# Kernel tuning notes

Hardware: AMD Instinct MI355X
Metric: run time of the kernel (lower is better)

The kernel has to match this reference:

```python
import jax, jax.numpy as jnp
from jax import lax
import numpy as np

BN_EPS = 1e-5

def nearest_resize(x, out_h, out_w):
    # torch F.interpolate(mode='nearest'): src = floor(dst * in / out)
    B, C, H, W = x.shape
    hi = (jnp.arange(out_h) * H) // out_h
    wi = (jnp.arange(out_w) * W) // out_w
    return x[:, :, hi][:, :, :, wi]

def conv1x1(x, w, b=None):
    y = jnp.einsum('bchw,oc->bohw', x, w)
    if b is not None:
        y = y + b[None, :, None, None]
    return y

def dwconv(x, w, stride, pad):
    C = x.shape[1]
    return lax.conv_general_dilated(x, w, (stride, stride), [(pad, pad), (pad, pad)],
                                    dimension_numbers=('NCHW', 'OIHW', 'NCHW'),
                                    feature_group_count=C)

def bn(x, g, b, m, v):
    scale = g / jnp.sqrt(v + BN_EPS)
    return (x - m[None, :, None, None]) * scale[None, :, None, None] + b[None, :, None, None]


def setup_inputs() -> dict:
    key = jax.random.key(0)
    ks = jax.random.split(key, 8)
    B, C, H0, W0 = 4, 512, 192, 192
    w_scale = 0.05
    return {
        'x': jax.random.normal(ks[0], (B, C, H0, W0), jnp.float32),
        'q_w': jax.random.normal(ks[1], (C, C), jnp.float32) * w_scale,
        'q_b': jnp.zeros((C,), jnp.float32),
        'kv_w': jax.random.normal(ks[2], (2 * C, C), jnp.float32) * w_scale,
        'kv_b': jnp.zeros((2 * C,), jnp.float32),
        'sr1_w': jax.random.normal(ks[3], (C, 1, 2, 2), jnp.float32) * w_scale,
        'bn1_g': jnp.ones((C,), jnp.float32),
        'bn1_b': jnp.zeros((C,), jnp.float32),
        'bn1_m': jnp.zeros((C,), jnp.float32),
        'bn1_v': jnp.ones((C,), jnp.float32),
        'sr2_w': jax.random.normal(ks[4], (C, C), jnp.float32) * w_scale,
        'bn2_g': jnp.ones((C,), jnp.float32),
        'bn2_b': jnp.zeros((C,), jnp.float32),
        'bn2_m': jnp.zeros((C,), jnp.float32),
        'bn2_v': jnp.ones((C,), jnp.float32),
        'lc_w': jax.random.normal(ks[5], (C, 1, 3, 3), jnp.float32) * w_scale,
        'lc_b': jnp.zeros((C,), jnp.float32),
        'head_num': 8,
    }


def reference(x, q_w, q_b, kv_w, kv_b, sr1_w, bn1_g, bn1_b, bn1_m, bn1_v,
              sr2_w, bn2_g, bn2_b, bn2_m, bn2_v, lc_w, lc_b, head_num):
    origin_h, origin_w = x.shape[2], x.shape[3]
    x = nearest_resize(x, origin_h // 4, origin_w // 4)
    B, C, H, W = x.shape
    hd = C // head_num
    scale = hd ** (-0.5)

    # q projection (1x1 conv with bias)
    q = conv1x1(x, q_w, q_b)  # [B,C,H,W]

    # spatial reduction: depthwise conv(k=sr, s=sr, p=sr//2) + BN + ReLU, then 1x1 + BN
    sr = sr1_w.shape[-1]
    kv = jax.nn.relu(bn(dwconv(x, sr1_w, sr, sr // 2), bn1_g, bn1_b, bn1_m, bn1_v))
    kv = bn(conv1x1(kv, sr2_w), bn2_g, bn2_b, bn2_m, bn2_v)

    # local depthwise 3x3 conv residual
    kv = dwconv(kv, lc_w, 1, 1) + lc_b[None, :, None, None] + kv

    # kv projection (1x1 conv, 2C output)
    kv = conv1x1(kv, kv_w, kv_b)
    k, v = jnp.split(kv, 2, axis=1)  # each [B,C,Hs,Ws]
    M = k.shape[2] * k.shape[3]

    q_ = jnp.swapaxes(q.reshape(B, head_num, hd, H * W), -1, -2)  # [B,h,N,hd]
    k_ = k.reshape(B, head_num, hd, M)                             # [B,h,hd,M]
    v_ = jnp.swapaxes(v.reshape(B, head_num, hd, M), -1, -2)       # [B,h,M,hd]

    attn = jax.nn.softmax(jnp.matmul(q_, k_) * scale, axis=-1)     # [B,h,N,M]
    out = jnp.swapaxes(jnp.matmul(attn, v_), -1, -2).reshape(B, C, H, W)

    # NOTE: original torch code passes size=(origin_w, origin_h)
    out = nearest_resize(out, origin_w, origin_h)
    return out
```

## Files before the change

kernel.cpp:

```cpp
#include <hip/hip_runtime.h>

#define Bsz 4
#define Cc  512
#define C2  1024
#define H0c 192
#define Hh  48
#define Nn  2304
#define HNh 8
#define HD  64
#define Hs  25
#define Ms  625

typedef const float* fp;
typedef _Float16 f16;
typedef __attribute__((ext_vector_type(8))) _Float16 f16x8;
typedef __attribute__((ext_vector_type(4))) _Float16 f16x4;
typedef __attribute__((ext_vector_type(4))) float    f32x4;

__global__ __launch_bounds__(256) void k_front(
    fp __restrict__ x, f16* __restrict__ xt, f16* __restrict__ kv1t,
    fp __restrict__ w1, fp g, fp bb, fp bm, fp bv,
    fp __restrict__ q_w, fp __restrict__ sr2_w, fp __restrict__ kv_w,
    f16* __restrict__ wh)
{
    __shared__ float tile[32][33];
    const int t = threadIdx.x;
    int bid = blockIdx.x;

    if (bid < 4608) {
        const int b  = bid / 1152;
        const int yi = (bid / 72) % 16;
        const int xi = bid % 72;
        const int s0 = xi * 32, r0 = yi * 32;
        const float* xb = x + (size_t)b * Cc * H0c * H0c;
        #pragma unroll
        for (int p = 0; p < 4; p++) {
            int e = t + p * 256; int i = e >> 5, j = e & 31;
            int c = r0 + i, n = s0 + j;
            tile[i][j] = xb[((size_t)c * H0c + (n / Hh) * 4) * H0c + (n % Hh) * 4];
        }
        __syncthreads();
        #pragma unroll
        for (int p = 0; p < 4; p++) {
            int e = t + p * 256; int oi = e >> 5, oj = e & 31;
            xt[((size_t)b * Nn + s0 + oi) * Cc + r0 + oj] = (f16)tile[oj][oi];
        }
    } else if (bid < 5888) {
        bid -= 4608;
        const int b  = bid / 320;
        const int yi = (bid / 20) % 16;
        const int xi = bid % 20;
        const int s0 = xi * 32, r0 = yi * 32;
        #pragma unroll
        for (int p = 0; p < 4; p++) {
            int e = t + p * 256; int i = e >> 5, j = e & 31;
            int c = r0 + i, n = s0 + j;
            float v = 0.f;
            if (n < Ms) {
                int ho = n / Hs, wo = n % Hs;
                const float* src = x + (size_t)(b * Cc + c) * H0c * H0c;
                float acc = 0.f;
                #pragma unroll
                for (int di = 0; di < 2; di++) {
                    int ih = ho * 2 - 1 + di;
                    if (ih < 0 || ih >= Hh) continue;
                    #pragma unroll
                    for (int dj = 0; dj < 2; dj++) {
                        int iw = wo * 2 - 1 + dj;
                        if (iw < 0 || iw >= Hh) continue;
                        acc += w1[c * 4 + di * 2 + dj] * src[(size_t)(ih * 4) * H0c + iw * 4];
                    }
                }
                float sc = g[c] * rsqrtf(bv[c] + 1e-5f);
                v = fmaxf((acc - bm[c]) * sc + bb[c], 0.f);
            }
            tile[i][j] = v;
        }
        __syncthreads();
        #pragma unroll
        for (int p = 0; p < 4; p++) {
            int e = t + p * 256; int oi = e >> 5, oj = e & 31;
            if (s0 + oi < Ms)
                kv1t[((size_t)b * Ms + s0 + oi) * Cc + r0 + oj] = (f16)tile[oj][oi];
        }
    } else {
        bid -= 5888;
        int i4 = (bid * 256 + t) * 4;
        float4 v;
        if (i4 < 262144)      v = *(const float4*)&q_w[i4];
        else if (i4 < 524288) v = *(const float4*)&sr2_w[i4 - 262144];
        else                  v = *(const float4*)&kv_w[i4 - 524288];
        f16x4 h; h[0] = (f16)v.x; h[1] = (f16)v.y; h[2] = (f16)v.z; h[3] = (f16)v.w;
        *(f16x4*)&wh[i4] = h;
    }
}

__global__ __launch_bounds__(256) void k_lct(const float* __restrict__ kv2,
                                             fp __restrict__ w, fp __restrict__ lb,
                                             f16* __restrict__ kv3t) {
    __shared__ float tile[32][33];
    const int b = blockIdx.z;
    const int s0 = blockIdx.x * 32, r0 = blockIdx.y * 32;
    const int t = threadIdx.x;
    #pragma unroll
    for (int p = 0; p < 4; p++) {
        int e = t + p * 256; int i = e >> 5, j = e & 31;
        int c = r0 + i, n = s0 + j;
        float v = 0.f;
        if (n < Ms) {
            int ho = n / Hs, wo = n % Hs;
            const float* src = kv2 + ((size_t)b * Cc + c) * Ms;
            float acc = 0.f;
            #pragma unroll
            for (int di = 0; di < 3; di++) {
                int ih = ho - 1 + di;
                if (ih < 0 || ih >= Hs) continue;
                #pragma unroll
                for (int dj = 0; dj < 3; dj++) {
                    int iw = wo - 1 + dj;
                    if (iw < 0 || iw >= Hs) continue;
                    acc += w[c * 9 + di * 3 + dj] * src[ih * Hs + iw];
                }
            }
            v = acc + lb[c] + src[n];
        }
        tile[i][j] = v;
    }
    __syncthreads();
    #pragma unroll
    for (int p = 0; p < 4; p++) {
        int e = t + p * 256; int oi = e >> 5, oj = e & 31;
        if (s0 + oi < Ms)
            kv3t[((size_t)b * Ms + s0 + oi) * Cc + r0 + oj] = (f16)tile[oj][oi];
    }
}

__device__ __forceinline__ void gemm_body(
    const f16* __restrict__ W, const f16* __restrict__ Xt,
    float* __restrict__ Yf, f16* __restrict__ Yt, f16* __restrict__ Vt,
    const int Md, const int Nd, const int NtRows, const int mode, const float oscale,
    fp __restrict__ bias,
    fp __restrict__ bn_g, fp __restrict__ bn_b, fp __restrict__ bn_m, fp __restrict__ bn_v,
    const int bx, const int by, const int bz, f16* sA, f16* sB)
{
    const int b  = bz;
    const int m0 = by * 128, n0 = bx * 128;
    const int t = threadIdx.x;
    const int lane = t & 63, w = t >> 6;
    const int lm = lane & 15, q = lane >> 4;
    const int wm = w >> 1, wn = w & 1;
    const f16* Xb = Xt + (size_t)b * Nd * 512;

    f32x4 acc[4][4];
    #pragma unroll
    for (int i = 0; i < 4; i++)
        #pragma unroll
        for (int j = 0; j < 4; j++)
            #pragma unroll
            for (int r = 0; r < 4; r++) acc[i][j][r] = 0.f;

    for (int k0 = 0; k0 < 512; k0 += 64) {
        {
            int r = t >> 1, hh = (t & 1) * 32;
            const f16* wr = W + (size_t)(m0 + r) * 512 + k0 + hh;
            f16* dst = &sA[r * 80 + hh];
            #pragma unroll
            for (int i = 0; i < 4; i++)
                *(f16x8*)&dst[i * 8] = *(const f16x8*)&wr[i * 8];
        }
        {
            int r = t >> 1, hh = (t & 1) * 32;
            bool ok = (n0 + r) < Nd;
            const f16* xr = Xb + (size_t)(n0 + r) * 512 + k0 + hh;
            f16* dst = &sB[r * 80 + hh];
            #pragma unroll
            for (int i = 0; i < 4; i++) {
                f16x8 v;
                if (ok) {
                    v = *(const f16x8*)&xr[i * 8];
                } else {
                    for (int z = 0; z < 8; z++) v[z] = (f16)0.f;
                }
                *(f16x8*)&dst[i * 8] = v;
            }
        }
        __syncthreads();
        #pragma unroll
        for (int ks = 0; ks < 2; ks++) {
            f16x8 af[4], bf[4];
            #pragma unroll
            for (int i = 0; i < 4; i++)
                af[i] = *(const f16x8*)&sA[(wm * 64 + i * 16 + lm) * 80 + ks * 32 + q * 8];
            #pragma unroll
            for (int j = 0; j < 4; j++)
                bf[j] = *(const f16x8*)&sB[(wn * 64 + j * 16 + lm) * 80 + ks * 32 + q * 8];
            #pragma unroll
            for (int i = 0; i < 4; i++)
                #pragma unroll
                for (int j = 0; j < 4; j++)
                    acc[i][j] = __builtin_amdgcn_mfma_f32_16x16x32_f16(af[i], bf[j], acc[i][j], 0, 0, 0);
        }
        __syncthreads();
    }

    #pragma unroll
    for (int i = 0; i < 4; i++) {
        int ob = m0 + wm * 64 + i * 16 + q * 4;
        float badd[4], bsc[4], bsh[4];
        #pragma unroll
        for (int r = 0; r < 4; r++) {
            int o = ob + r;
            badd[r] = bias ? bias[o] : 0.f;
            if (bn_g) { bsc[r] = bn_g[o] * rsqrtf(bn_v[o] + 1e-5f); bsh[r] = bn_b[o] - bn_m[o] * bsc[r]; }
            else      { bsc[r] = 1.f; bsh[r] = 0.f; }
        }
        #pragma unroll
        for (int j = 0; j < 4; j++) {
            int n = n0 + wn * 64 + j * 16 + lm;
            f32x4 a = acc[i][j];
            if (mode == 0) {
                if (n < Nd) {
                    #pragma unroll
                    for (int r = 0; r < 4; r++)
                        Yf[((size_t)b * Md + ob + r) * Nd + n] = (a[r] + badd[r]) * bsc[r] + bsh[r];
                }
            } else if (mode == 1 || (mode == 2 && ob < 512)) {
                f16x4 h;
                #pragma unroll
                for (int r = 0; r < 4; r++) h[r] = (f16)((a[r] + badd[r]) * oscale);
                int hh = ob >> 6, d0 = ob & 63;
                *(f16x4*)&Yt[((size_t)(b * 8 + hh) * NtRows + n) * 64 + d0] = h;
            } else {
                #pragma unroll
                for (int r = 0; r < 4; r++) {
                    float val = (n < Nd) ? (a[r] + badd[r]) : 0.f;
                    Vt[((size_t)b * Cc + (ob + r - 512)) * 640 + n] = (f16)val;
                }
            }
        }
    }
}

__global__ __launch_bounds__(256) void k_gemm_mfma(
    const f16* __restrict__ W, const f16* __restrict__ Xt,
    float* __restrict__ Yf, f16* __restrict__ Yt, f16* __restrict__ Vt,
    const int Md, const int Nd, const int NtRows, const int mode, const float oscale,
    fp __restrict__ bias,
    fp __restrict__ bn_g, fp __restrict__ bn_b, fp __restrict__ bn_m, fp __restrict__ bn_v)
{
    __shared__ f16 sA[128 * 80];
    __shared__ f16 sB[128 * 80];
    gemm_body(W, Xt, Yf, Yt, Vt, Md, Nd, NtRows, mode, oscale,
              bias, bn_g, bn_b, bn_m, bn_v,
              blockIdx.x, blockIdx.y, blockIdx.z, sA, sB);
}

__global__ __launch_bounds__(256) void k_gemm2(
    const f16* __restrict__ W0, const f16* __restrict__ X0, f16* __restrict__ Yt0,
    const float osc0, fp __restrict__ bias0,
    const f16* __restrict__ W1, const f16* __restrict__ X1, float* __restrict__ Yf1,
    fp g1, fp b1, fp m1, fp v1)
{
    __shared__ f16 sA[128 * 80];
    __shared__ f16 sB[128 * 80];
    int bid = blockIdx.x;
    if (bid < 288) {
        int bx = bid % 18, by = (bid / 18) % 4, bz = bid / 72;
        gemm_body(W0, X0, nullptr, Yt0, nullptr, Cc, Nn, Nn, 1, osc0,
                  bias0, nullptr, nullptr, nullptr, nullptr, bx, by, bz, sA, sB);
    } else {
        bid -= 288;
        int bx = bid % 5, by = (bid / 5) % 4, bz = bid / 20;
        gemm_body(W1, X1, Yf1, nullptr, nullptr, Cc, Ms, 0, 0, 1.f,
                  nullptr, g1, b1, m1, v1, bx, by, bz, sA, sB);
    }
}

__global__ __launch_bounds__(256) void k_attn_mfma(
    const f16* __restrict__ Qt, const f16* __restrict__ Kt,
    const f16* __restrict__ Vt, float* __restrict__ Obuf)
{
    __shared__ f16 sK[64 * 80];
    __shared__ f16 sV[64 * 80];
    __shared__ f16 sP[4][16 * 80];

    int bh = blockIdx.y;
    int n0 = blockIdx.x * 64;
    int t = threadIdx.x, w = t >> 6, lane = t & 63;
    int lm = lane & 15, q = lane >> 4;
    f16* sPw = &sP[w][0];

    f16x8 qf[2];
    {
        const f16* qrow = Qt + ((size_t)bh * Nn + n0 + w * 16 + lm) * 64;
        qf[0] = *(const f16x8*)&qrow[q * 8];
        qf[1] = *(const f16x8*)&qrow[32 + q * 8];
    }

    f32x4 od[4];
    #pragma unroll
    for (int dt = 0; dt < 4; dt++)
        #pragma unroll
        for (int r = 0; r < 4; r++) od[dt][r] = 0.f;
    float mold[4], lold[4];
    #pragma unroll
    for (int r = 0; r < 4; r++) { mold[r] = -1e30f; lold[r] = 0.f; }

    int kr = t >> 2, kc = t & 3;
    const f16* kbase = Kt + (size_t)bh * 640 * 64;
    const f16* vbase = Vt + (size_t)bh * 64 * 640;

    for (int mc = 0; mc < 640; mc += 64) {
        {
            const f16* ksrc = kbase + (size_t)(mc + kr) * 64;
            *(f16x8*)&sK[kr * 80 + kc * 8]      = *(const f16x8*)&ksrc[kc * 8];
            *(f16x8*)&sK[kr * 80 + 32 + kc * 8] = *(const f16x8*)&ksrc[32 + kc * 8];
            const f16* vsrc = vbase + (size_t)kr * 640 + mc;
            *(f16x8*)&sV[kr * 80 + kc * 8]      = *(const f16x8*)&vsrc[kc * 8];
            *(f16x8*)&sV[kr * 80 + 32 + kc * 8] = *(const f16x8*)&vsrc[32 + kc * 8];
        }
        __syncthreads();

        f32x4 sc4[4];
        #pragma unroll
        for (int j = 0; j < 4; j++)
            #pragma unroll
            for (int r = 0; r < 4; r++) sc4[j][r] = 0.f;
        #pragma unroll
        for (int ks = 0; ks < 2; ks++) {
            #pragma unroll
            for (int j = 0; j < 4; j++) {
                f16x8 kf = *(const f16x8*)&sK[(j * 16 + lm) * 80 + ks * 32 + q * 8];
                sc4[j] = __builtin_amdgcn_mfma_f32_16x16x32_f16(qf[ks], kf, sc4[j], 0, 0, 0);
            }
        }

        const bool lastc = (mc >= 576);
        #pragma unroll
        for (int reg = 0; reg < 4; reg++) {
            float mx;
            if (lastc) {
                mx = -1e30f;
                #pragma unroll
                for (int j = 0; j < 4; j++) {
                    float s = sc4[j][reg];
                    if (576 + j * 16 + lm >= Ms) s = -1e30f;
                    sc4[j][reg] = s;
                    mx = fmaxf(mx, s);
                }
            } else {
                mx = fmaxf(fmaxf(sc4[0][reg], sc4[1][reg]),
                           fmaxf(sc4[2][reg], sc4[3][reg]));
            }
            #pragma unroll
            for (int off = 1; off < 16; off <<= 1) mx = fmaxf(mx, __shfl_xor(mx, off));
            float mnew = fmaxf(mold[reg], mx);
            float alpha = __expf(mold[reg] - mnew);
            float rs = 0.f;
            #pragma unroll
            for (int j = 0; j < 4; j++) {
                float p = __expf(sc4[j][reg] - mnew);
                sc4[j][reg] = p;
                rs += p;
            }
            #pragma unroll
            for (int off = 1; off < 16; off <<= 1) rs += __shfl_xor(rs, off);
            lold[reg] = lold[reg] * alpha + rs;
            mold[reg] = mnew;
            #pragma unroll
            for (int dt = 0; dt < 4; dt++) od[dt][reg] *= alpha;
            #pragma unroll
            for (int j = 0; j < 4; j++)
                sPw[(q * 4 + reg) * 80 + j * 16 + lm] = (f16)sc4[j][reg];
        }

        #pragma unroll
        for (int ks = 0; ks < 2; ks++) {
            f16x8 pa = *(const f16x8*)&sPw[lm * 80 + ks * 32 + q * 8];
            #pragma unroll
            for (int dt = 0; dt < 4; dt++) {
                f16x8 vf = *(const f16x8*)&sV[(dt * 16 + lm) * 80 + ks * 32 + q * 8];
                od[dt] = __builtin_amdgcn_mfma_f32_16x16x32_f16(pa, vf, od[dt], 0, 0, 0);
            }
        }
        __syncthreads();
    }

    float inv[4];
    #pragma unroll
    for (int r = 0; r < 4; r++) inv[r] = 1.f / lold[r];
    #pragma unroll
    for (int dt = 0; dt < 4; dt++) {
        f32x4 o;
        #pragma unroll
        for (int r = 0; r < 4; r++) o[r] = od[dt][r] * inv[r];
        size_t c = (size_t)bh * 64 + dt * 16 + lm;
        *(f32x4*)&Obuf[c * Nn + n0 + w * 16 + q * 4] = o;
    }
}

__global__ __launch_bounds__(256) void k_upsample(const float* __restrict__ O,
                                                  float* __restrict__ out) {
    const size_t total = (size_t)Bsz * Cc * H0c * 48;
    for (size_t idx = (size_t)blockIdx.x * 256 + threadIdx.x; idx < total;
         idx += (size_t)gridDim.x * 256) {
        int jg = (int)(idx % 48);
        int i  = (int)((idx / 48) % H0c);
        int bc = (int)(idx / ((size_t)48 * H0c));
        float s = O[(size_t)bc * Nn + (i >> 2) * Hh + jg];
        float4 pack = make_float4(s, s, s, s);
        *(float4*)(out + ((size_t)bc * H0c + i) * H0c + jg * 4) = pack;
    }
}

extern "C" void kernel_launch(void* const* d_in, const int* in_sizes, int n_in,
                              void* d_out, int out_size, void* d_ws, size_t ws_size,
                              hipStream_t stream) {
    (void)in_sizes; (void)n_in; (void)out_size; (void)ws_size;
    fp x     = (fp)d_in[0];
    fp q_w   = (fp)d_in[1];
    fp q_b   = (fp)d_in[2];
    fp kv_w  = (fp)d_in[3];
    fp kv_b  = (fp)d_in[4];
    fp sr1_w = (fp)d_in[5];
    fp bn1_g = (fp)d_in[6];
    fp bn1_b = (fp)d_in[7];
    fp bn1_m = (fp)d_in[8];
    fp bn1_v = (fp)d_in[9];
    fp sr2_w = (fp)d_in[10];
    fp bn2_g = (fp)d_in[11];
    fp bn2_b = (fp)d_in[12];
    fp bn2_m = (fp)d_in[13];
    fp bn2_v = (fp)d_in[14];
    fp lc_w  = (fp)d_in[15];
    fp lc_b  = (fp)d_in[16];
    float* out = (float*)d_out;

    float* ws   = (float*)d_ws;
    f16*   xt   = (f16*)ws;
    f16*   kv1t = (f16*)(ws + 2359296);
    f16*   wh   = (f16*)(ws + 2999296);
    float* kv2  = ws + 3523584;
    float* Obuf = ws;
    f16*   Qt   = (f16*)(ws + 4803584);
    f16*   Kt   = (f16*)(ws + 7162880);
    f16*   vt   = (f16*)(ws + 7818240);
    f16*   kv3t = (f16*)(ws + 8473600);

    k_front<<<6912, 256, 0, stream>>>(x, xt, kv1t, sr1_w, bn1_g, bn1_b, bn1_m, bn1_v,
                                      q_w, sr2_w, kv_w, wh);
    k_gemm2<<<368, 256, 0, stream>>>(wh, xt, Qt, 0.125f, q_b,
                                     wh + 262144, kv1t, kv2, bn2_g, bn2_b, bn2_m, bn2_v);
    k_lct<<<dim3(20, 16, Bsz), 256, 0, stream>>>(kv2, lc_w, lc_b, kv3t);
    k_gemm_mfma<<<dim3(5, 8, Bsz), 256, 0, stream>>>(wh + 524288, kv3t, nullptr, Kt, vt,
        C2, Ms, 640, 2, 1.f, kv_b, nullptr, nullptr, nullptr, nullptr);
    k_attn_mfma<<<dim3(Nn / 64, Bsz * HNh), 256, 0, stream>>>(Qt, Kt, vt, Obuf);
    k_upsample<<<2048, 256, 0, stream>>>(Obuf, out);
}
```

Baseline: 603.2 us.

## Fuse nearest upsample into attention epilogue and prefetch GEMM tiles in registers

The attention kernel now stages its normalized output tile in shared memory, reusing the K/V/P buffers, and writes the 4x4 nearest-upsampled result straight to the final output. This removes the intermediate Obuf round trip and the separate upsample launch. Separately, the GEMM body prefetches the next K-slice of A and B into registers while the MFMAs run on the current slice, hiding global load latency. The cost is higher register pressure in the GEMM and a heavier, store-bound epilogue in the attention kernel.

```diff
diff --git a/kernel.cpp b/kernel.cpp
--- a/kernel.cpp
+++ b/kernel.cpp
@@ -151,6 +151,13 @@
     const int wm = w >> 1, wn = w & 1;
     const f16* Xb = Xt + (size_t)b * Nd * 512;
 
+    const int sr = t >> 1, shh = (t & 1) * 32;
+    const f16* wrow = W + (size_t)(m0 + sr) * 512 + shh;
+    const bool okB  = (n0 + sr) < Nd;
+    const f16* xrow = Xb + (size_t)(n0 + sr) * 512 + shh;
+    f16* dstA = &sA[sr * 80 + shh];
+    f16* dstB = &sB[sr * 80 + shh];
+
     f32x4 acc[4][4];
     #pragma unroll
     for (int i = 0; i < 4; i++)
@@ -159,32 +166,30 @@
             #pragma unroll
             for (int r = 0; r < 4; r++) acc[i][j][r] = 0.f;
 
+    f16x8 ra[4], rb[4];
+    #pragma unroll
+    for (int i = 0; i < 4; i++) {
+        ra[i] = *(const f16x8*)&wrow[i * 8];
+        if (okB) rb[i] = *(const f16x8*)&xrow[i * 8];
+        else     for (int z = 0; z < 8; z++) rb[i][z] = (f16)0.f;
+    }
+
     for (int k0 = 0; k0 < 512; k0 += 64) {
-        {
-            int r = t >> 1, hh = (t & 1) * 32;
-            const f16* wr = W + (size_t)(m0 + r) * 512 + k0 + hh;
-            f16* dst = &sA[r * 80 + hh];
-            #pragma unroll
-            for (int i = 0; i < 4; i++)
-                *(f16x8*)&dst[i * 8] = *(const f16x8*)&wr[i * 8];
-        }
-        {
-            int r = t >> 1, hh = (t & 1) * 32;
-            bool ok = (n0 + r) < Nd;
-            const f16* xr = Xb + (size_t)(n0 + r) * 512 + k0 + hh;
-            f16* dst = &sB[r * 80 + hh];
+        #pragma unroll
+        for (int i = 0; i < 4; i++) {
+            *(f16x8*)&dstA[i * 8] = ra[i];
+            *(f16x8*)&dstB[i * 8] = rb[i];
+        }
+        __syncthreads();
+        if (k0 + 64 < 512) {
+            const f16* wn_ = wrow + k0 + 64;
+            const f16* xn_ = xrow + k0 + 64;
             #pragma unroll
             for (int i = 0; i < 4; i++) {
-                f16x8 v;
-                if (ok) {
-                    v = *(const f16x8*)&xr[i * 8];
-                } else {
-                    for (int z = 0; z < 8; z++) v[z] = (f16)0.f;
-                }
-                *(f16x8*)&dst[i * 8] = v;
-            }
-        }
-        __syncthreads();
+                ra[i] = *(const f16x8*)&wn_[i * 8];
+                if (okB) rb[i] = *(const f16x8*)&xn_[i * 8];
+            }
+        }
         #pragma unroll
         for (int ks = 0; ks < 2; ks++) {
             f16x8 af[4], bf[4];
@@ -278,17 +283,19 @@
 
 __global__ __launch_bounds__(256) void k_attn_mfma(
     const f16* __restrict__ Qt, const f16* __restrict__ Kt,
-    const f16* __restrict__ Vt, float* __restrict__ Obuf)
+    const f16* __restrict__ Vt, float* __restrict__ out)
 {
-    __shared__ f16 sK[64 * 80];
-    __shared__ f16 sV[64 * 80];
-    __shared__ f16 sP[4][16 * 80];
+    __shared__ __align__(16) unsigned char smem[30720];
+    f16* sK = (f16*)smem;
+    f16* sV = (f16*)(smem + 10240);
+    f16* sP4 = (f16*)(smem + 20480);
+    float* sO = (float*)smem;
 
     int bh = blockIdx.y;
     int n0 = blockIdx.x * 64;
     int t = threadIdx.x, w = t >> 6, lane = t & 63;
     int lm = lane & 15, q = lane >> 4;
-    f16* sPw = &sP[w][0];
+    f16* sPw = sP4 + w * (16 * 80);
 
     f16x8 qf[2];
     {
@@ -394,22 +401,23 @@
         f32x4 o;
         #pragma unroll
         for (int r = 0; r < 4; r++) o[r] = od[dt][r] * inv[r];
-        size_t c = (size_t)bh * 64 + dt * 16 + lm;
-        *(f32x4*)&Obuf[c * Nn + n0 + w * 16 + q * 4] = o;
-    }
-}
-
-__global__ __launch_bounds__(256) void k_upsample(const float* __restrict__ O,
-                                                  float* __restrict__ out) {
-    const size_t total = (size_t)Bsz * Cc * H0c * 48;
-    for (size_t idx = (size_t)blockIdx.x * 256 + threadIdx.x; idx < total;
-         idx += (size_t)gridDim.x * 256) {
-        int jg = (int)(idx % 48);
-        int i  = (int)((idx / 48) % H0c);
-        int bc = (int)(idx / ((size_t)48 * H0c));
-        float s = O[(size_t)bc * Nn + (i >> 2) * Hh + jg];
-        float4 pack = make_float4(s, s, s, s);
-        *(float4*)(out + ((size_t)bc * H0c + i) * H0c + jg * 4) = pack;
+        *(f32x4*)&sO[(dt * 16 + lm) * 68 + w * 16 + q * 4] = o;
+    }
+    __syncthreads();
+
+    const int bq = bh >> 3, hch = (bh & 7) * 64;
+    const int nl = lane;
+    const int n  = n0 + nl;
+    const int orow = (n / Hh) * 4, ocol = (n % Hh) * 4;
+    #pragma unroll
+    for (int it = 0; it < 16; it++) {
+        int c = w * 16 + it;
+        float s = sO[c * 68 + nl];
+        float* oc = out + ((size_t)(bq * Cc + hch + c) * H0c + orow) * H0c + ocol;
+        float4 pk = make_float4(s, s, s, s);
+        #pragma unroll
+        for (int ii = 0; ii < 4; ii++)
+            *(float4*)&oc[ii * H0c] = pk;
     }
 }
 
@@ -441,7 +449,6 @@
     f16*   kv1t = (f16*)(ws + 2359296);
     f16*   wh   = (f16*)(ws + 2999296);
     float* kv2  = ws + 3523584;
-    float* Obuf = ws;
     f16*   Qt   = (f16*)(ws + 4803584);
     f16*   Kt   = (f16*)(ws + 7162880);
     f16*   vt   = (f16*)(ws + 7818240);
@@ -454,6 +461,5 @@
     k_lct<<<dim3(20, 16, Bsz), 256, 0, stream>>>(kv2, lc_w, lc_b, kv3t);
     k_gemm_mfma<<<dim3(5, 8, Bsz), 256, 0, stream>>>(wh + 524288, kv3t, nullptr, Kt, vt,
         C2, Ms, 640, 2, 1.f, kv_b, nullptr, nullptr, nullptr, nullptr);
-    k_attn_mfma<<<dim3(Nn / 64, Bsz * HNh), 256, 0, stream>>>(Qt, Kt, vt, Obuf);
-    k_upsample<<<2048, 256, 0, stream>>>(Obuf, out);
-}
+    k_attn_mfma<<<dim3(Nn / 64, Bsz * HNh), 256, 0, stream>>>(Qt, Kt, vt, out);
+}
```

Result: faster. 577.1 us (-4.3%).
